# Performance work log

Hardware: AMD Instinct MI355X
Metric: run time of the kernel (lower is better)

The kernel has to match this reference:

```python
import jax, jax.numpy as jnp
import numpy as np

EPS = 1e-9
P, Dp, D, Dd, ITERS = 6, 8, 4, 12, 2


def squash(v, axis=-1):
    s2 = jnp.sum(v * v, axis=axis, keepdims=True)
    return s2 / (1.0 + s2) * v / (jnp.sqrt(s2) + EPS)


def setup_inputs() -> dict:
    key = jax.random.key(0)
    kx, kwp, kw = jax.random.split(key, 3)
    B, L, C, K = 64, 1024, 128, 6
    X = jax.random.normal(kx, (B, L, C, K), dtype=jnp.float32)
    # primary linear: Linear(C -> P*Dp)
    Wp = jax.random.normal(kwp, (P * Dp, C), dtype=jnp.float32) * (1.0 / np.sqrt(C))
    bp = jnp.zeros((P * Dp,), dtype=jnp.float32)
    # routing weights W: [K, D, Dd, P*Dp], xavier-uniform scale
    lim = np.sqrt(6.0 / (Dd + P * Dp))
    W = jax.random.uniform(kw, (K, D, Dd, P * Dp), dtype=jnp.float32, minval=-lim, maxval=lim)
    return {"X": X, "Wp": Wp, "bp": bp, "W": W}


def reference(X, Wp, bp, W):
    B, L, C, K = X.shape
    # primary projection: [B,L,K,C] @ [C, P*Dp]
    Xk = jnp.transpose(X, (0, 1, 3, 2))            # [B,L,K,C]
    Xp = jnp.einsum('blkc,pc->blkp', Xk, Wp) + bp   # [B,L,K,P*Dp]
    Xp = squash(Xp.reshape(B, L, K, P, Dp), axis=-1).reshape(B, L, K, P * Dp)
    # prediction vectors u_hat: [B,L,K,D,Dd]
    u_hat = jnp.einsum('kdqp,blkp->blkdq', W, Xp)
    # dynamic routing
    b = jnp.zeros((B, L, K, D), dtype=X.dtype)
    v = None
    for _ in range(ITERS):
        c = jax.nn.softmax(b, axis=-1)                     # over D
        s = jnp.einsum('blkd,blkdq->bldq', c, u_hat)       # sum over K
        v = squash(s, axis=-1)                             # [B,L,D,Dd]
        b = b + jnp.einsum('blkdq,bldq->blkd', u_hat, v)
    return v.reshape(B, L, D * Dd)
```

## Files before the change

kernel.cpp:

```cpp
#include <hip/hip_runtime.h>
#include <hip/hip_bf16.h>
#include <math.h>

#define EPSQ 1e-9f

typedef float  floatx4 __attribute__((ext_vector_type(4)));
typedef short  short8  __attribute__((ext_vector_type(8)));
typedef unsigned short u16;
typedef unsigned int   u32;

constexpr int TP  = 16;
constexpr int SA  = 40;
constexpr int SS  = 49;
constexpr int SA2 = 48;


__device__ __forceinline__ float fast_rcp(float x)  { return __builtin_amdgcn_rcpf(x); }
__device__ __forceinline__ float fast_sqrt(float x) { return __builtin_amdgcn_sqrtf(x); }

__device__ __forceinline__ float squash_rf(float s2) {
    return s2 * fast_rcp(1.0f + s2) * fast_rcp(fast_sqrt(s2) + EPSQ);
}

__device__ __forceinline__ void cvt_hilo(float a, float b, u32& hi, u32& lo) {
    __hip_bfloat162 h = __float22bfloat162_rn(make_float2(a, b));
    float2 hf = __bfloat1622float2(h);
    __hip_bfloat162 l = __float22bfloat162_rn(make_float2(a - hf.x, b - hf.y));
    __builtin_memcpy(&hi, &h, 4);
    __builtin_memcpy(&lo, &l, 4);
}

__device__ __forceinline__ float g16sum(float x) {
    x += __shfl_xor(x, 1);
    x += __shfl_xor(x, 2);
    x += __shfl_xor(x, 4);
    x += __shfl_xor(x, 8);
    return x;
}

__device__ __forceinline__ float g8sum(float x) {
    x += __shfl_xor(x, 1);
    x += __shfl_xor(x, 2);
    x += __shfl_xor(x, 4);
    return x;
}

__device__ __forceinline__ void route_and_write(float u0, float u1, float u2,
                                                float u3, float u4, float u5,
                                                int d, int q, bool act,
                                                float* __restrict__ out, long pos)
{
    float s = (u0 + u1 + u2 + u3 + u4 + u5) * 0.25f;
    float s2 = g16sum(s * s);
    float v = s * squash_rf(s2);

    float ss = 0.f;
#define ROUTE_K(UK)                                        \
    {                                                      \
        float b = g16sum((UK) * v);                        \
        float mm = fmaxf(b, __shfl_xor(b, 16));            \
        mm = fmaxf(mm, __shfl_xor(mm, 32));                \
        float e = __expf(b - mm);                          \
        float es = e + __shfl_xor(e, 16);                  \
        es += __shfl_xor(es, 32);                          \
        ss = fmaf(e * fast_rcp(es), (UK), ss);             \
    }
    ROUTE_K(u0) ROUTE_K(u1) ROUTE_K(u2) ROUTE_K(u3) ROUTE_K(u4) ROUTE_K(u5)
#undef ROUTE_K
    float ss2 = g16sum(ss * ss);
    float vv = ss * squash_rf(ss2);
    if (act) out[pos * 48 + d * 12 + q] = vv;
}

__global__ void prep_kernel(const float* __restrict__ Wp, const float* __restrict__ W,
                            u16* __restrict__ wpf, u16* __restrict__ wf) {
    int gid = blockIdx.x * 256 + threadIdx.x;
    int stride = gridDim.x * 256;
    for (int i = gid; i < 12288; i += stride) {
        int j = i & 7, lane = (i >> 3) & 63, kc = (i >> 9) & 3, vt = i >> 11;
        int var = (vt >= 3) ? 1 : 0;
        int ct = vt - 3 * var;
        int p = ct * 16 + (lane & 15);
        int c = kc * 32 + (lane >> 4) * 8 + j;
        float x = Wp[p * 128 + c];
        __hip_bfloat16 hb = __float2bfloat16(x);
        if (var) { float hf = __bfloat162float(hb); hb = __float2bfloat16(x - hf); }
        u16 u; __builtin_memcpy(&u, &hb, 2);
        wpf[i] = u;
    }
    for (int i = gid; i < 36864; i += stride) {
        int j = i & 7, lane = (i >> 3) & 63, kc = (i >> 9) & 1, q3 = i >> 10;
        int ct = q3 % 3, kk = q3 / 3;
        int k = kk % 6, var = kk / 6;
        int dq = ct * 16 + (lane & 15);
        int p = kc * 32 + (lane >> 4) * 8 + j;
        float x = (p < 48) ? W[(k * 48 + dq) * 48 + p] : 0.f;
        __hip_bfloat16 hb = __float2bfloat16(x);
        if (var) { float hf = __bfloat162float(hb); hb = __float2bfloat16(x - hf); }
        u16 u; __builtin_memcpy(&u, &hb, 2);
        wf[i] = u;
    }
}

__global__ __launch_bounds__(256, 6)
void capsule_kernel(
    const float* __restrict__ X,
    const float* __restrict__ bp,
    const u16* __restrict__ wpf,
    const u16* __restrict__ wf,
    float* __restrict__ out)
{
    __shared__ __align__(16) char raw[18848];
    u16*   sAh  = (u16*)raw;
    u16*   sAl  = sAh + 96 * SA;
    u16*   sA2h = (u16*)raw;
    u16*   sA2l = sA2h + 96 * SA2;
    float* sU   = (float*)raw;
    const u16* zpad = (const u16*)(raw + 18816);

    const int t    = threadIdx.x;
    const int lane = t & 63;
    const int w    = t >> 6;
    const int m    = lane & 15;
    const int quad = lane >> 4;
    const long pos_base = (long)blockIdx.x * TP;

    if (t < 8) ((u32*)(raw + 18816))[t] = 0u;

    floatx4 acc_a = {0.f,0.f,0.f,0.f}, acc_b = {0.f,0.f,0.f,0.f}, acc_c = {0.f,0.f,0.f,0.f},
            acc_d = {0.f,0.f,0.f,0.f}, acc_e = {0.f,0.f,0.f,0.f};

#define S1_TILE(ACC, TI)                                                              \
    { int T = w + 4 * (TI);                                                           \
      if (T < 18) {                                                                   \
        int rt = T / 3, ct = T - 3 * rt;                                              \
        short8 ah = *(const short8*)(sAh + (rt * 16 + m) * SA + quad * 8);            \
        short8 al = *(const short8*)(sAl + (rt * 16 + m) * SA + quad * 8);            \
        short8 bh = *(const short8*)(wpf + ((ct * 4 + kc) * 64 + lane) * 8);          \
        short8 bl = *(const short8*)(wpf + (((3 + ct) * 4 + kc) * 64 + lane) * 8);    \
        ACC = __builtin_amdgcn_mfma_f32_16x16x32_bf16(ah, bh, ACC, 0, 0, 0);          \
        ACC = __builtin_amdgcn_mfma_f32_16x16x32_bf16(ah, bl, ACC, 0, 0, 0);          \
        ACC = __builtin_amdgcn_mfma_f32_16x16x32_bf16(al, bh, ACC, 0, 0, 0);          \
      } }

    #pragma unroll
    for (int kc = 0; kc < 4; ++kc) {
        if (kc > 0) __syncthreads();
        {
            int pos = t >> 4, cp = t & 15;
            const float4* src = (const float4*)(X + (pos_base + pos) * 768 + kc * 192) + cp * 3;
            float4 f0 = src[0], f1 = src[1], f2 = src[2];
            u16* bh = sAh + (pos * 6) * SA + cp * 2;
            u16* bl = sAl + (pos * 6) * SA + cp * 2;
            u32 h, l;
            cvt_hilo(f0.x, f1.z, h, l); *(u32*)(bh + 0 * SA) = h; *(u32*)(bl + 0 * SA) = l;
            cvt_hilo(f0.y, f1.w, h, l); *(u32*)(bh + 1 * SA) = h; *(u32*)(bl + 1 * SA) = l;
            cvt_hilo(f0.z, f2.x, h, l); *(u32*)(bh + 2 * SA) = h; *(u32*)(bl + 2 * SA) = l;
            cvt_hilo(f0.w, f2.y, h, l); *(u32*)(bh + 3 * SA) = h; *(u32*)(bl + 3 * SA) = l;
            cvt_hilo(f1.x, f2.z, h, l); *(u32*)(bh + 4 * SA) = h; *(u32*)(bl + 4 * SA) = l;
            cvt_hilo(f1.y, f2.w, h, l); *(u32*)(bh + 5 * SA) = h; *(u32*)(bl + 5 * SA) = l;
        }
        __syncthreads();
        S1_TILE(acc_a, 0) S1_TILE(acc_b, 1) S1_TILE(acc_c, 2) S1_TILE(acc_d, 3) S1_TILE(acc_e, 4)
    }
#undef S1_TILE
    __syncthreads();

#define FUSE_ONE(V)                                                   \
    { float val = (V) + bv;                                           \
      float s2 = g8sum(val * val);                                    \
      float sv = val * squash_rf(s2);                                 \
      __hip_bfloat16 hb = __float2bfloat16(sv);                       \
      float hf = __bfloat162float(hb);                                \
      __hip_bfloat16 lb = __float2bfloat16(sv - hf);                  \
      u16 hu, lu;                                                     \
      __builtin_memcpy(&hu, &hb, 2); __builtin_memcpy(&lu, &lb, 2);   \
      int dr = (kk * 16 + pp) * SA2 + ct * 16 + m;                    \
      sA2h[dr] = hu; sA2l[dr] = lu; }

#define S1_FUSE(ACC, TI)                                              \
    { int T = w + 4 * (TI);                                           \
      if (T < 18) {                                                   \
        int rt = T / 3, ct = T - 3 * rt;                              \
        float bv = bp[ct * 16 + m];                                   \
        int row0 = rt * 16 + quad * 4;                                \
        int pp = row0 / 6, kk = row0 - 6 * pp;                        \
        FUSE_ONE(ACC.x)                                               \
        kk++; if (kk == 6) { kk = 0; pp++; }                          \
        FUSE_ONE(ACC.y)                                               \
        kk++; if (kk == 6) { kk = 0; pp++; }                          \
        FUSE_ONE(ACC.z)                                               \
        kk++; if (kk == 6) { kk = 0; pp++; }                          \
        FUSE_ONE(ACC.w)                                               \
      } }
    S1_FUSE(acc_a, 0) S1_FUSE(acc_b, 1) S1_FUSE(acc_c, 2) S1_FUSE(acc_d, 3) S1_FUSE(acc_e, 4)
#undef S1_FUSE
#undef FUSE_ONE
    __syncthreads();

    floatx4 uacc_a = {0.f,0.f,0.f,0.f}, uacc_b = {0.f,0.f,0.f,0.f}, uacc_c = {0.f,0.f,0.f,0.f},
            uacc_d = {0.f,0.f,0.f,0.f}, uacc_e = {0.f,0.f,0.f,0.f};

#define S2_TILE(ACC, TI)                                                                      \
    { int T = w + 4 * (TI);                                                                   \
      if (T < 18) {                                                                           \
        int k = T / 3, ct = T - 3 * k;                                                        \
        const u16* arh = sA2h + (k * 16 + m) * SA2;                                           \
        const u16* arl = sA2l + (k * 16 + m) * SA2;                                           \
        {                                                                                     \
          short8 ah0 = *(const short8*)(arh + quad * 8);                                      \
          short8 al0 = *(const short8*)(arl + quad * 8);                                      \
          short8 bh0 = *(const short8*)(wf + (((k * 3 + ct) * 2 + 0) * 64 + lane) * 8);       \
          short8 bl0 = *(const short8*)(wf + ((((6 + k) * 3 + ct) * 2 + 0) * 64 + lane) * 8); \
          ACC = __builtin_amdgcn_mfma_f32_16x16x32_bf16(ah0, bh0, ACC, 0, 0, 0);              \
          ACC = __builtin_amdgcn_mfma_f32_16x16x32_bf16(ah0, bl0, ACC, 0, 0, 0);              \
          ACC = __builtin_amdgcn_mfma_f32_16x16x32_bf16(al0, bh0, ACC, 0, 0, 0);              \
        }                                                                                     \
        {                                                                                     \
          const u16* a1h = (quad < 2) ? (arh + 32 + quad * 8) : zpad;                         \
          const u16* a1l = (quad < 2) ? (arl + 32 + quad * 8) : zpad;                         \
          short8 ah1 = *(const short8*)a1h;                                                   \
          short8 al1 = *(const short8*)a1l;                                                   \
          short8 bh1 = *(const short8*)(wf + (((k * 3 + ct) * 2 + 1) * 64 + lane) * 8);       \
          short8 bl1 = *(const short8*)(wf + ((((6 + k) * 3 + ct) * 2 + 1) * 64 + lane) * 8); \
          ACC = __builtin_amdgcn_mfma_f32_16x16x32_bf16(ah1, bh1, ACC, 0, 0, 0);              \
          ACC = __builtin_amdgcn_mfma_f32_16x16x32_bf16(ah1, bl1, ACC, 0, 0, 0);              \
          ACC = __builtin_amdgcn_mfma_f32_16x16x32_bf16(al1, bh1, ACC, 0, 0, 0);              \
        }                                                                                     \
      } }
    S2_TILE(uacc_a, 0) S2_TILE(uacc_b, 1) S2_TILE(uacc_c, 2) S2_TILE(uacc_d, 3) S2_TILE(uacc_e, 4)
#undef S2_TILE
    __syncthreads();

#define S2_EPI(ACC, TI)                                                   \
    { int T = w + 4 * (TI);                                               \
      if (T < 18) {                                                       \
        int k = T / 3, ct = T - 3 * k;                                    \
        sU[((quad * 4 + 0) * 6 + k) * SS + ct * 16 + m] = ACC.x;          \
        sU[((quad * 4 + 1) * 6 + k) * SS + ct * 16 + m] = ACC.y;          \
        sU[((quad * 4 + 2) * 6 + k) * SS + ct * 16 + m] = ACC.z;          \
        sU[((quad * 4 + 3) * 6 + k) * SS + ct * 16 + m] = ACC.w;          \
      } }
    S2_EPI(uacc_a, 0) S2_EPI(uacc_b, 1) S2_EPI(uacc_c, 2) S2_EPI(uacc_d, 3) S2_EPI(uacc_e, 4)
#undef S2_EPI
    __syncthreads();

    const int d = lane >> 4;
    const int q = lane & 15;
    const bool act = (q < 12);
    const int dqi = d * 12 + (act ? q : 0);

    #pragma unroll
    for (int i = 0; i < 4; ++i) {
        int pos = w * 4 + i;
        const float* u = sU + (pos * 6) * SS + dqi;
        float a0 = u[0 * SS], a1 = u[1 * SS], a2 = u[2 * SS];
        float a3 = u[3 * SS], a4 = u[4 * SS], a5 = u[5 * SS];
        if (!act) { a0 = a1 = a2 = a3 = a4 = a5 = 0.f; }
        route_and_write(a0, a1, a2, a3, a4, a5, d, q, act, out, pos_base + pos);
    }
}

extern "C" void kernel_launch(void* const* d_in, const int* in_sizes, int n_in,
                              void* d_out, int out_size, void* d_ws, size_t ws_size,
                              hipStream_t stream) {
    const float* X  = (const float*)d_in[0];
    const float* Wp = (const float*)d_in[1];
    const float* bp = (const float*)d_in[2];
    const float* W  = (const float*)d_in[3];
    float* out = (float*)d_out;

    u16* wpf = (u16*)d_ws;
    u16* wf  = wpf + 12288;

    hipLaunchKernelGGL(prep_kernel, dim3(48), dim3(256), 0, stream, Wp, W, wpf, wf);

    const int n_pos = 64 * 1024;
    hipLaunchKernelGGL(capsule_kernel, dim3(n_pos / TP), dim3(256), 0, stream,
                       X, bp, wpf, wf, out);
}
```

Before: 330.0 us.

## Prefetch next X chunk into registers and use LDS-only barriers

Unrolls the four K-chunks of the primary projection and issues the global loads for the next chunk before the current chunk's convert, barrier and MFMA phase, double-buffering X in registers. It also replaces __syncthreads with a barrier that waits only on LDS counters (lgkmcnt), so in-flight global loads are not drained at each barrier. The aim is to hide global memory latency behind compute. In exchange it uses more registers, which may cut occupancy.

```diff
diff --git a/kernel.cpp b/kernel.cpp
--- a/kernel.cpp
+++ b/kernel.cpp
@@ -14,6 +14,12 @@
 constexpr int SS  = 49;
 constexpr int SA2 = 48;
 
+
+#define BAR_LGKM() do {                                          \
+    asm volatile("s_waitcnt lgkmcnt(0)" ::: "memory");           \
+    __builtin_amdgcn_s_barrier();                                \
+    asm volatile("" ::: "memory");                               \
+} while (0)
 
 __device__ __forceinline__ float fast_rcp(float x)  { return __builtin_amdgcn_rcpf(x); }
 __device__ __forceinline__ float fast_sqrt(float x) { return __builtin_amdgcn_sqrtf(x); }
@@ -130,41 +136,64 @@
     floatx4 acc_a = {0.f,0.f,0.f,0.f}, acc_b = {0.f,0.f,0.f,0.f}, acc_c = {0.f,0.f,0.f,0.f},
             acc_d = {0.f,0.f,0.f,0.f}, acc_e = {0.f,0.f,0.f,0.f};
 
-#define S1_TILE(ACC, TI)                                                              \
+    const int posS = t >> 4, cp = t & 15;
+    const float4* xsrc = (const float4*)(X + (pos_base + posS) * 768) + cp * 3;
+    u16* wbh = sAh + (posS * 6) * SA + cp * 2;
+    u16* wbl = sAl + (posS * 6) * SA + cp * 2;
+
+#define CVT_WRITE(F0, F1, F2)                                                                 \
+    {   u32 h, l;                                                                             \
+        cvt_hilo(F0.x, F1.z, h, l); *(u32*)(wbh + 0 * SA) = h; *(u32*)(wbl + 0 * SA) = l;     \
+        cvt_hilo(F0.y, F1.w, h, l); *(u32*)(wbh + 1 * SA) = h; *(u32*)(wbl + 1 * SA) = l;     \
+        cvt_hilo(F0.z, F2.x, h, l); *(u32*)(wbh + 2 * SA) = h; *(u32*)(wbl + 2 * SA) = l;     \
+        cvt_hilo(F0.w, F2.y, h, l); *(u32*)(wbh + 3 * SA) = h; *(u32*)(wbl + 3 * SA) = l;     \
+        cvt_hilo(F1.x, F2.z, h, l); *(u32*)(wbh + 4 * SA) = h; *(u32*)(wbl + 4 * SA) = l;     \
+        cvt_hilo(F1.y, F2.w, h, l); *(u32*)(wbh + 5 * SA) = h; *(u32*)(wbl + 5 * SA) = l;     \
+    }
+
+#define S1_TILE(ACC, TI, KC)                                                          \
     { int T = w + 4 * (TI);                                                           \
       if (T < 18) {                                                                   \
         int rt = T / 3, ct = T - 3 * rt;                                              \
         short8 ah = *(const short8*)(sAh + (rt * 16 + m) * SA + quad * 8);            \
         short8 al = *(const short8*)(sAl + (rt * 16 + m) * SA + quad * 8);            \
-        short8 bh = *(const short8*)(wpf + ((ct * 4 + kc) * 64 + lane) * 8);          \
-        short8 bl = *(const short8*)(wpf + (((3 + ct) * 4 + kc) * 64 + lane) * 8);    \
+        short8 bh = *(const short8*)(wpf + ((ct * 4 + (KC)) * 64 + lane) * 8);        \
+        short8 bl = *(const short8*)(wpf + (((3 + ct) * 4 + (KC)) * 64 + lane) * 8);  \
         ACC = __builtin_amdgcn_mfma_f32_16x16x32_bf16(ah, bh, ACC, 0, 0, 0);          \
         ACC = __builtin_amdgcn_mfma_f32_16x16x32_bf16(ah, bl, ACC, 0, 0, 0);          \
         ACC = __builtin_amdgcn_mfma_f32_16x16x32_bf16(al, bh, ACC, 0, 0, 0);          \
       } }
 
-    #pragma unroll
-    for (int kc = 0; kc < 4; ++kc) {
-        if (kc > 0) __syncthreads();
-        {
-            int pos = t >> 4, cp = t & 15;
-            const float4* src = (const float4*)(X + (pos_base + pos) * 768 + kc * 192) + cp * 3;
-            float4 f0 = src[0], f1 = src[1], f2 = src[2];
-            u16* bh = sAh + (pos * 6) * SA + cp * 2;
-            u16* bl = sAl + (pos * 6) * SA + cp * 2;
-            u32 h, l;
-            cvt_hilo(f0.x, f1.z, h, l); *(u32*)(bh + 0 * SA) = h; *(u32*)(bl + 0 * SA) = l;
-            cvt_hilo(f0.y, f1.w, h, l); *(u32*)(bh + 1 * SA) = h; *(u32*)(bl + 1 * SA) = l;
-            cvt_hilo(f0.z, f2.x, h, l); *(u32*)(bh + 2 * SA) = h; *(u32*)(bl + 2 * SA) = l;
-            cvt_hilo(f0.w, f2.y, h, l); *(u32*)(bh + 3 * SA) = h; *(u32*)(bl + 3 * SA) = l;
-            cvt_hilo(f1.x, f2.z, h, l); *(u32*)(bh + 4 * SA) = h; *(u32*)(bl + 4 * SA) = l;
-            cvt_hilo(f1.y, f2.w, h, l); *(u32*)(bh + 5 * SA) = h; *(u32*)(bl + 5 * SA) = l;
-        }
-        __syncthreads();
-        S1_TILE(acc_a, 0) S1_TILE(acc_b, 1) S1_TILE(acc_c, 2) S1_TILE(acc_d, 3) S1_TILE(acc_e, 4)
-    }
+#define S1_PHASE(KC)                                                         \
+    S1_TILE(acc_a, 0, KC) S1_TILE(acc_b, 1, KC) S1_TILE(acc_c, 2, KC)        \
+    S1_TILE(acc_d, 3, KC) S1_TILE(acc_e, 4, KC)
+
+    float4 fa0 = xsrc[0],   fa1 = xsrc[1],   fa2 = xsrc[2];
+    float4 fb0 = xsrc[48],  fb1 = xsrc[49],  fb2 = xsrc[50];
+    CVT_WRITE(fa0, fa1, fa2);
+    BAR_LGKM();
+    S1_PHASE(0)
+    BAR_LGKM();
+
+    fa0 = xsrc[96];  fa1 = xsrc[97];  fa2 = xsrc[98];
+    CVT_WRITE(fb0, fb1, fb2);
+    BAR_LGKM();
+    S1_PHASE(1)
+    BAR_LGKM();
+
+    fb0 = xsrc[144]; fb1 = xsrc[145]; fb2 = xsrc[146];
+    CVT_WRITE(fa0, fa1, fa2);
+    BAR_LGKM();
+    S1_PHASE(2)
+    BAR_LGKM();
+
+    CVT_WRITE(fb0, fb1, fb2);
+    BAR_LGKM();
+    S1_PHASE(3)
+    BAR_LGKM();
+#undef S1_PHASE
 #undef S1_TILE
-    __syncthreads();
+#undef CVT_WRITE
 
 #define FUSE_ONE(V)                                                   \
     { float val = (V) + bv;                                           \
@@ -196,7 +225,7 @@
     S1_FUSE(acc_a, 0) S1_FUSE(acc_b, 1) S1_FUSE(acc_c, 2) S1_FUSE(acc_d, 3) S1_FUSE(acc_e, 4)
 #undef S1_FUSE
 #undef FUSE_ONE
-    __syncthreads();
+    BAR_LGKM();
 
     floatx4 uacc_a = {0.f,0.f,0.f,0.f}, uacc_b = {0.f,0.f,0.f,0.f}, uacc_c = {0.f,0.f,0.f,0.f},
             uacc_d = {0.f,0.f,0.f,0.f}, uacc_e = {0.f,0.f,0.f,0.f};
@@ -230,7 +259,7 @@
       } }
     S2_TILE(uacc_a, 0) S2_TILE(uacc_b, 1) S2_TILE(uacc_c, 2) S2_TILE(uacc_d, 3) S2_TILE(uacc_e, 4)
 #undef S2_TILE
-    __syncthreads();
+    BAR_LGKM();
 
 #define S2_EPI(ACC, TI)                                                   \
     { int T = w + 4 * (TI);                                               \
@@ -243,7 +272,7 @@
       } }
     S2_EPI(uacc_a, 0) S2_EPI(uacc_b, 1) S2_EPI(uacc_c, 2) S2_EPI(uacc_d, 3) S2_EPI(uacc_e, 4)
 #undef S2_EPI
-    __syncthreads();
+    BAR_LGKM();
 
     const int d = lane >> 4;
     const int q = lane & 15;
```

Result: no change. 325.4 us (-1.4%).
